# Performance work log

Hardware: AMD Instinct MI355X
Metric: run time of the kernel (lower is better)

## Reference

```python
import jax, jax.numpy as jnp
import numpy as np

B, N, S, DIM, H = 128, 8, 16, 64, 4
DH = DIM // H

def setup_inputs() -> dict:
    key = jax.random.key(0)
    ks = jax.random.split(key, 10)
    return {
        "self_embeddings": jax.random.normal(ks[0], (B, N, DIM), jnp.float32),
        "ngh_user_embeddings": jax.random.normal(ks[1], (B, S, DIM), jnp.float32),
        "ngh_entity_embeddings": jax.random.normal(ks[2], (B, N, S, DIM), jnp.float32),
        "user_embeddings": jax.random.normal(ks[3], (B, DIM), jnp.float32),
        "item_embeddings": jax.random.normal(ks[4], (B, DIM), jnp.float32),
        "W_r": jax.random.normal(ks[5], (B, N, S, DIM, DIM), jnp.float32) * 0.1,
        "W_ui": jax.random.normal(ks[6], (DIM, DIM), jnp.float32) * 0.1,
        "lin_W": jax.random.normal(ks[7], (DIM, DIM), jnp.float32) * 0.1,
        "lin_b": jnp.zeros((DIM,), jnp.float32),
        "linUI_W": jax.random.normal(ks[8], (DIM, DIM), jnp.float32) * 0.1,
        "linUI_b": jnp.zeros((DIM,), jnp.float32),
        "is_item_layer": 1,
    }

def reference(self_embeddings, ngh_user_embeddings, ngh_entity_embeddings,
              user_embeddings, item_embeddings, W_r, W_ui,
              lin_W, lin_b, linUI_W, linUI_b, is_item_layer):
    scale = 1.0 / np.sqrt(float(DH))
    # ---- user-side ego embedding (agg_type='sum') ----
    # Wi[b,i] = sum_j W_ui[i,j] * item[b,j]
    Wi = item_embeddings @ W_ui.T                          # [B, DIM]
    Wi_h = Wi.reshape(B, H, DH)                            # split heads (chunks of DH)
    nghu_h = ngh_user_embeddings.reshape(B, S, H, DH)
    att_u = jnp.einsum('bhd,bshd->bhs', Wi_h, nghu_h) * scale
    att_u = jax.nn.softmax(att_u, axis=-1)                 # softmax over S
    user_ego = jnp.einsum('bhs,bshd->bhd', att_u, nghu_h).reshape(B, DIM)
    # sum-agg + linear_UI + act (dropout is identity at inference)
    item_UI = jax.nn.relu((item_embeddings + user_ego) @ linUI_W.T + linUI_b)  # [B, DIM]
    # ---- entity-side ego embedding (repr_type='sum') ----
    signal = user_embeddings + item_UI                     # [B, DIM]
    v = signal[:, None, :] * self_embeddings               # [B, N, DIM]
    # q[b,n,s,i] = sum_j W_r[b,n,s,i,j] * v[b,n,j]
    q = jnp.einsum('bnsij,bnj->bnsi', W_r, v)              # [B, N, S, DIM]
    q_h = q.reshape(B, N, S, H, DH)
    nghe_h = ngh_entity_embeddings.reshape(B, N, S, H, DH)
    att_e = jnp.einsum('bnshd,bnshd->bnhs', q_h, nghe_h) * scale
    att_e = jax.nn.softmax(att_e, axis=-1)                 # softmax over S
    entity_ego = jnp.einsum('bnhs,bnshd->bnhd', att_e, nghe_h).reshape(B, N, DIM)
    # ---- final aggregation (is_item_layer=True, agg_type='sum') ----
    agg = self_embeddings + user_ego[:, None, :] + entity_ego
    out = jax.nn.relu(agg @ lin_W.T + lin_b)               # [B, N, DIM]
    return out
```

## Files before the change

kernel.cpp:

```cpp
#include <hip/hip_runtime.h>
#include <hip/hip_bf16.h>

#define B_   128
#define N_   8
#define S_   16
#define DIM_ 64
#define H_   4
#define DH_  16

__device__ __forceinline__ float dot_row64f(const float* __restrict__ row,
                                            const float* __restrict__ v) {
    const float4* rp = (const float4*)row;
    float acc = 0.f;
#pragma unroll
    for (int m = 0; m < 16; ++m) {
        float4 u = rp[m];
        acc = fmaf(u.x, v[4 * m + 0], acc);
        acc = fmaf(u.y, v[4 * m + 1], acc);
        acc = fmaf(u.z, v[4 * m + 2], acc);
        acc = fmaf(u.w, v[4 * m + 3], acc);
    }
    return acc;
}

__global__ __launch_bounds__(256) void EntityAggregator_63342177681721_kernel(
    const float* __restrict__ self_e,
    const float* __restrict__ nghu,
    const float* __restrict__ nghe,
    const float* __restrict__ user_e,
    const float* __restrict__ item_e,
    const float* __restrict__ W_r,
    const float* __restrict__ W_ui,
    const float* __restrict__ lin_W,
    const float* __restrict__ lin_b,
    const float* __restrict__ linUI_W,
    const float* __restrict__ linUI_b,
    float* __restrict__ out)
{
    const int blk = blockIdx.x;
    const int b   = blk >> 3;
    const int t   = threadIdx.x;

    __shared__ float sU[S_][DIM_ + 1];
    __shared__ float sE[S_][DIM_ + 1];
    __shared__ float sQ[S_][DIM_ + 1];
    __shared__ float sItem[DIM_];
    __shared__ float sWi[DIM_];
    __shared__ float sAtt[H_][S_];
    __shared__ float sUei[DIM_];
    __shared__ float sTi[DIM_];
    __shared__ float sV[DIM_];
    __shared__ float sAgg[DIM_];

    {
        const int e0 = t * 4;
        const int s  = e0 >> 6;
        const int c  = e0 & 63;
        float4 uu = *(const float4*)(nghu + (size_t)b * S_ * DIM_ + e0);
        sU[s][c + 0] = uu.x; sU[s][c + 1] = uu.y;
        sU[s][c + 2] = uu.z; sU[s][c + 3] = uu.w;
        float4 ee = *(const float4*)(nghe + (size_t)blk * S_ * DIM_ + e0);
        sE[s][c + 0] = ee.x; sE[s][c + 1] = ee.y;
        sE[s][c + 2] = ee.z; sE[s][c + 3] = ee.w;
        if (t < DIM_) sItem[t] = item_e[(size_t)b * DIM_ + t];
    }
    __syncthreads();

    if (t < DIM_) sWi[t] = dot_row64f(W_ui + t * DIM_, sItem);
    __syncthreads();

    if (t < DIM_) {
        const int h = t >> 4, s = t & 15;
        float l = 0.f;
#pragma unroll
        for (int d = 0; d < DH_; ++d) l = fmaf(sWi[h * DH_ + d], sU[s][h * DH_ + d], l);
        l *= 0.25f;
        float mx = l;
#pragma unroll
        for (int off = 8; off; off >>= 1) mx = fmaxf(mx, __shfl_xor(mx, off, 16));
        float e = __expf(l - mx);
        float sm = e;
#pragma unroll
        for (int off = 8; off; off >>= 1) sm += __shfl_xor(sm, off, 16);
        sAtt[h][s] = e / sm;
    }
    __syncthreads();

    if (t < DIM_) {
        const int h = t >> 4;
        float ego = 0.f;
#pragma unroll
        for (int s = 0; s < S_; ++s) ego = fmaf(sAtt[h][s], sU[s][t], ego);
        sUei[t] = ego;
        sTi[t]  = sItem[t] + ego;
    }
    __syncthreads();

    if (t < DIM_) {
        float a   = dot_row64f(linUI_W + t * DIM_, sTi) + linUI_b[t];
        float iui = fmaxf(a, 0.f);
        float sig = user_e[(size_t)b * DIM_ + t] + iui;
        sV[t] = sig * self_e[(size_t)blk * DIM_ + t];
    }
    __syncthreads();

    {
        float v[DIM_];
#pragma unroll
        for (int j = 0; j < DIM_; ++j) v[j] = sV[j];
        const float* Wp = W_r + (size_t)blk * (S_ * DIM_ * DIM_);
#pragma unroll
        for (int k = 0; k < 4; ++k) {
            const int r = t + 256 * k;
            const float4* rp = (const float4*)(Wp + (size_t)r * DIM_);
            float acc = 0.f;
#pragma unroll
            for (int m = 0; m < 16; ++m) {
                float4 u = rp[m];
                acc = fmaf(u.x, v[4 * m + 0], acc);
                acc = fmaf(u.y, v[4 * m + 1], acc);
                acc = fmaf(u.z, v[4 * m + 2], acc);
                acc = fmaf(u.w, v[4 * m + 3], acc);
            }
            sQ[r >> 6][r & 63] = acc;
        }
    }
    __syncthreads();

    if (t < DIM_) {
        const int h = t >> 4, s = t & 15;
        float l = 0.f;
#pragma unroll
        for (int d = 0; d < DH_; ++d) l = fmaf(sQ[s][h * DH_ + d], sE[s][h * DH_ + d], l);
        l *= 0.25f;
        float mx = l;
#pragma unroll
        for (int off = 8; off; off >>= 1) mx = fmaxf(mx, __shfl_xor(mx, off, 16));
        float e = __expf(l - mx);
        float sm = e;
#pragma unroll
        for (int off = 8; off; off >>= 1) sm += __shfl_xor(sm, off, 16);
        sAtt[h][s] = e / sm;
    }
    __syncthreads();

    if (t < DIM_) {
        const int h = t >> 4;
        float ego = 0.f;
#pragma unroll
        for (int s = 0; s < S_; ++s) ego = fmaf(sAtt[h][s], sE[s][t], ego);
        sAgg[t] = self_e[(size_t)blk * DIM_ + t] + sUei[t] + ego;
    }
    __syncthreads();

    if (t < DIM_) {
        float o = dot_row64f(lin_W + t * DIM_, sAgg) + lin_b[t];
        o = fmaxf(o, 0.f);
        out[(size_t)blk * DIM_ + t] = o;
    }
}

extern "C" void kernel_launch(void* const* d_in, const int* in_sizes, int n_in,
                              void* d_out, int out_size, void* d_ws, size_t ws_size,
                              hipStream_t stream) {
    (void)in_sizes; (void)n_in; (void)d_ws; (void)ws_size; (void)out_size;
    const float* self_e  = (const float*)d_in[0];
    const float* nghu    = (const float*)d_in[1];
    const float* nghe    = (const float*)d_in[2];
    const float* user_e  = (const float*)d_in[3];
    const float* item_e  = (const float*)d_in[4];
    const float* W_r     = (const float*)d_in[5];
    const float* W_ui    = (const float*)d_in[6];
    const float* lin_W   = (const float*)d_in[7];
    const float* lin_b   = (const float*)d_in[8];
    const float* linUI_W = (const float*)d_in[9];
    const float* linUI_b = (const float*)d_in[10];

    dim3 grid(B_ * N_);
    dim3 block(256);
    hipLaunchKernelGGL(EntityAggregator_63342177681721_kernel, grid, block, 0, stream,
                       self_e, nghu, nghe, user_e, item_e, W_r, W_ui,
                       lin_W, lin_b, linUI_W, linUI_b, (float*)d_out);
}
```

Baseline: 415.9 us.

## Stream W_r into double-buffered LDS with async global-to-LDS loads

Each block's W_r slice is now copied straight into two 32 KB shared-memory buffers with `global_load_lds`. The first two chunks are issued at kernel entry so they overlap the user-side attention prelude, and later chunks are prefetched one ahead while the current one is consumed. The matvec is reorganised so two threads share a row, read a rotated column order to avoid LDS bank conflicts, and combine partial sums with a shuffle. This hides the latency of the large W_r stream. In exchange the block uses much more LDS, which limits blocks per CU, and it adds a barrier per chunk.

Result: faster. 380.6 us (-8.5%).

```diff
diff --git a/kernel.cpp b/kernel.cpp
--- a/kernel.cpp
+++ b/kernel.cpp
@@ -21,6 +21,13 @@
         acc = fmaf(u.w, v[4 * m + 3], acc);
     }
     return acc;
+}
+
+__device__ __forceinline__ void load_lds16(const float* g, float* lds) {
+    __builtin_amdgcn_global_load_lds(
+        (const __attribute__((address_space(1))) void*)g,
+        (__attribute__((address_space(3))) void*)lds,
+        16, 0, 0);
 }
 
 __global__ __launch_bounds__(256) void EntityAggregator_63342177681721_kernel(
@@ -37,10 +44,14 @@
     const float* __restrict__ linUI_b,
     float* __restrict__ out)
 {
-    const int blk = blockIdx.x;
-    const int b   = blk >> 3;
-    const int t   = threadIdx.x;
-
+    const int blk  = blockIdx.x;
+    const int b    = blk >> 3;
+    const int t    = threadIdx.x;
+    const int w    = t >> 6;
+    const int lane = t & 63;
+
+    __shared__ __align__(16) float sW0[128 * DIM_];
+    __shared__ __align__(16) float sW1[128 * DIM_];
     __shared__ float sU[S_][DIM_ + 1];
     __shared__ float sE[S_][DIM_ + 1];
     __shared__ float sQ[S_][DIM_ + 1];
@@ -49,8 +60,21 @@
     __shared__ float sAtt[H_][S_];
     __shared__ float sUei[DIM_];
     __shared__ float sTi[DIM_];
-    __shared__ float sV[DIM_];
+    __shared__ __align__(16) float sV[DIM_];
     __shared__ float sAgg[DIM_];
+
+    const float* Wp = W_r + (size_t)blk * (S_ * DIM_ * DIM_);
+
+    {
+        const float* g0 = Wp + w * 256 + lane * 4;
+#pragma unroll
+        for (int rr = 0; rr < 8; ++rr)
+            load_lds16(g0 + rr * 1024, sW0 + w * 256 + rr * 1024);
+        const float* g1 = Wp + 8192 + w * 256 + lane * 4;
+#pragma unroll
+        for (int rr = 0; rr < 8; ++rr)
+            load_lds16(g1 + rr * 1024, sW1 + w * 256 + rr * 1024);
+    }
 
     {
         const int e0 = t * 4;
@@ -105,27 +129,39 @@
     __syncthreads();
 
     {
-        float v[DIM_];
-#pragma unroll
-        for (int j = 0; j < DIM_; ++j) v[j] = sV[j];
-        const float* Wp = W_r + (size_t)blk * (S_ * DIM_ * DIM_);
-#pragma unroll
-        for (int k = 0; k < 4; ++k) {
-            const int r = t + 256 * k;
-            const float4* rp = (const float4*)(Wp + (size_t)r * DIM_);
+        const int  row  = t >> 1;
+        const int  half = t & 1;
+        const float4* vv4 = (const float4*)sV;
+#pragma unroll 1
+        for (int c = 0; c < 8; ++c) {
+            if (c >= 1 && c < 7) {
+                float* nb = ((c + 1) & 1) ? sW1 : sW0;
+                const float* g = Wp + (size_t)(c + 1) * 8192 + w * 256 + lane * 4;
+#pragma unroll
+                for (int rr = 0; rr < 8; ++rr)
+                    load_lds16(g + rr * 1024, nb + w * 256 + rr * 1024);
+            }
+            const float4* bp = (const float4*)((c & 1) ? sW1 : sW0);
             float acc = 0.f;
 #pragma unroll
-            for (int m = 0; m < 16; ++m) {
-                float4 u = rp[m];
-                acc = fmaf(u.x, v[4 * m + 0], acc);
-                acc = fmaf(u.y, v[4 * m + 1], acc);
-                acc = fmaf(u.z, v[4 * m + 2], acc);
-                acc = fmaf(u.w, v[4 * m + 3], acc);
+            for (int m = 0; m < 8; ++m) {
+                const int mm   = (m + row) & 7;
+                const int col4 = half * 8 + mm;
+                float4 u = bp[row * 16 + col4];
+                float4 v = vv4[col4];
+                acc = fmaf(u.x, v.x, acc);
+                acc = fmaf(u.y, v.y, acc);
+                acc = fmaf(u.z, v.z, acc);
+                acc = fmaf(u.w, v.w, acc);
             }
-            sQ[r >> 6][r & 63] = acc;
+            acc += __shfl_xor(acc, 1);
+            if (half == 0) {
+                const int rg = c * 128 + row;
+                sQ[rg >> 6][rg & 63] = acc;
+            }
+            __syncthreads();
         }
     }
-    __syncthreads();
 
     if (t < DIM_) {
         const int h = t >> 4, s = t & 15;
```
